# Kernel optimization log

Measured on AMD Instinct MI355X. Metric: run time of the kernel, lower is better.

The kernel has to match this reference:

```python
import math
import jax, jax.numpy as jnp
import numpy as np

D_MODEL = 256
D2 = 2 * D_MODEL
NHEADS = 8
NLAYERS = 6
FFN = 1024
Q, B, S = 300, 16, 1024


def _ln(x, eps=1e-5):
    m = jnp.mean(x, axis=-1, keepdims=True)
    v = jnp.mean((x - m) ** 2, axis=-1, keepdims=True)
    return (x - m) / jnp.sqrt(v + eps)


def _mlp2(x, W1, b1, W2, b2):
    return jnp.maximum(x @ W1 + b1, 0.0) @ W2 + b2


def _sine_embed(pos, d_model):
    # pos: [Q, B, 2] -> [Q, B, d_model]
    fd = d_model // 2
    dim_t = jnp.arange(fd, dtype=jnp.float32)
    dim_t = 10000.0 ** (2.0 * jnp.floor(dim_t / 2.0) / fd)
    scale = 2.0 * math.pi
    px = (pos[:, :, 0] * scale)[:, :, None] / dim_t
    py = (pos[:, :, 1] * scale)[:, :, None] / dim_t

    def inter(p):
        q, b, _ = p.shape
        return jnp.stack((jnp.sin(p[:, :, 0::2]), jnp.cos(p[:, :, 1::2])), axis=3).reshape(q, b, -1)

    return jnp.concatenate((inter(py), inter(px)), axis=2)


def _pairwise_iou(b):
    # b: [B, Q, 4] xyxy -> [B, Q, Q]
    area = (b[..., 2] - b[..., 0]) * (b[..., 3] - b[..., 1])
    lt = jnp.maximum(b[:, :, None, :2], b[:, None, :, :2])
    rb = jnp.minimum(b[:, :, None, 2:], b[:, None, :, 2:])
    wh = jnp.clip(rb - lt, 0.0)
    inter = wh[..., 0] * wh[..., 1]
    union = area[:, :, None] + area[:, None, :] - inter
    return inter / union


def _mha(q, k, v, Wq, Wk, Wv, Wo, bias=None):
    # q: [L,B,D], k/v: [S,B,D]
    L, Bb, D = q.shape
    Ss = k.shape[0]
    hd = D // NHEADS
    qh = (q @ Wq).reshape(L, Bb, NHEADS, hd).transpose(1, 2, 0, 3)  # [B,H,L,hd]
    kh = (k @ Wk).reshape(Ss, Bb, NHEADS, hd).transpose(1, 2, 0, 3)
    vh = (v @ Wv).reshape(Ss, Bb, NHEADS, hd).transpose(1, 2, 0, 3)
    logits = jnp.einsum('bhqd,bhkd->bhqk', qh, kh) / jnp.sqrt(jnp.float32(hd))
    if bias is not None:
        logits = logits + bias[:, None]  # broadcast over heads
    a = jax.nn.softmax(logits, axis=-1)
    o = jnp.einsum('bhqk,bhkd->bhqd', a, vh).transpose(2, 0, 1, 3).reshape(L, Bb, D)
    return o @ Wo


def setup_inputs() -> dict:
    key = jax.random.key(0)
    ks = iter(jax.random.split(key, 40))
    f32 = jnp.float32
    d = D_MODEL
    sc = 0.02
    inp = {
        'tgt': jax.random.normal(next(ks), (Q, B, D2), f32),
        'memory': jax.random.normal(next(ks), (S, B, D2), f32),
        'pos': jax.random.normal(next(ks), (S, B, D2), f32),
        'query_pos': jax.random.normal(next(ks), (Q, B, d), f32),
        # query_scale MLP (d->d->d)
        'qs_W1': jax.random.normal(next(ks), (d, d), f32) * sc, 'qs_b1': jnp.zeros((d,), f32),
        'qs_W2': jax.random.normal(next(ks), (d, d), f32) * sc, 'qs_b2': jnp.zeros((d,), f32),
        # ref_point_head MLP (d->d->2)
        'rp_W1': jax.random.normal(next(ks), (d, d), f32) * sc, 'rp_b1': jnp.zeros((d,), f32),
        'rp_W2': jax.random.normal(next(ks), (d, 2), f32) * sc, 'rp_b2': jnp.zeros((2,), f32),
        # bbox_embed_func MLP (d->d->4)
        'bb_W1': jax.random.normal(next(ks), (d, d), f32) * sc, 'bb_b1': jnp.zeros((d,), f32),
        'bb_W2': jax.random.normal(next(ks), (d, 4), f32) * sc, 'bb_b2': jnp.zeros((4,), f32),
    }
    for name in ['sa_Wq', 'sa_Wk', 'sa_Wv', 'sa_Wo', 'ca_Wq', 'ca_Wk', 'ca_Wv', 'ca_Wo']:
        inp[name] = jax.random.normal(next(ks), (NLAYERS, D2, D2), f32) * sc
    inp['ff_W1'] = jax.random.normal(next(ks), (NLAYERS, D2, FFN), f32) * sc
    inp['ff_b1'] = jnp.zeros((NLAYERS, FFN), f32)
    inp['ff_W2'] = jax.random.normal(next(ks), (NLAYERS, FFN, D2), f32) * sc
    inp['ff_b2'] = jnp.zeros((NLAYERS, D2), f32)
    return inp


def reference(tgt, memory, pos, query_pos,
              qs_W1, qs_b1, qs_W2, qs_b2,
              rp_W1, rp_b1, rp_W2, rp_b2,
              bb_W1, bb_b1, bb_W2, bb_b2,
              sa_Wq, sa_Wk, sa_Wv, sa_Wo,
              ca_Wq, ca_Wk, ca_Wv, ca_Wo,
              ff_W1, ff_b1, ff_W2, ff_b2):
    d = D_MODEL
    output = tgt
    ref_before = _mlp2(query_pos, rp_W1, rp_b1, rp_W2, rp_b2)          # [Q,B,2]
    reference_points = jax.nn.sigmoid(ref_before).transpose(1, 0, 2)   # [B,Q,2]
    qp2 = jnp.concatenate((query_pos, query_pos), axis=-1)             # [Q,B,2d]
    for l in range(NLAYERS):
        obj_center = reference_points.transpose(1, 0, 2)               # [Q,B,2]
        pos_transform = _mlp2(output[..., d:], qs_W1, qs_b1, qs_W2, qs_b2)
        qs = _sine_embed(obj_center, d) * pos_transform                # [Q,B,d]
        tmp = _mlp2(output[..., d:], bb_W1, bb_b1, bb_W2, bb_b2)       # [Q,B,4]
        tmp = tmp.at[..., :2].add(ref_before)
        coord = jax.nn.sigmoid(tmp)                                    # cxcywh
        cx, cy, w, h = coord[..., 0], coord[..., 1], coord[..., 2], coord[..., 3]
        boxes = jnp.stack((cx - 0.5 * w, cy - 0.5 * h, cx + 0.5 * w, cy + 0.5 * h),
                          axis=-1).transpose(1, 0, 2)                  # [B,Q,4]
        gious = jax.lax.stop_gradient(_pairwise_iou(boxes))            # [B,Q,Q]
        cs = (cx + cy).transpose(1, 0)                                 # [B,Q]
        cxcys = jax.lax.stop_gradient((cs[:, :, None] > cs[:, None, :]).astype(output.dtype))
        bias = gious + cxcys                                            # [B,Q,Q]
        qs2 = jnp.concatenate((qs, qs), axis=-1)                        # [Q,B,2d]
        # self-attention with giou/cxcy bias
        qsa = output + qp2
        sa = _mha(qsa, qsa, output, sa_Wq[l], sa_Wk[l], sa_Wv[l], sa_Wo[l], bias=bias)
        output = _ln(output + sa)
        # cross-attention, sine-modulated query
        ca = _mha(output + qp2 + qs2, memory + pos, memory,
                  ca_Wq[l], ca_Wk[l], ca_Wv[l], ca_Wo[l])
        output = _ln(output + ca)
        ff = jnp.maximum(output @ ff_W1[l] + ff_b1[l], 0.0) @ ff_W2[l] + ff_b2[l]
        output = _ln(output + ff)
    return output[None]  # [1,Q,B,2d]
```

## Files before the change

kernel.cpp:

```cpp
#include <hip/hip_runtime.h>
#include <cmath>

#define QLEN 300
#define BATCH 16
#define SLEN 1024
#define DM 256
#define DD 512
#define FFND 1024
#define NQROWS (QLEN*BATCH)
#define NMROWS (SLEN*BATCH)
#define LQPAD 304
#define SAKPAD 320

typedef __attribute__((ext_vector_type(8))) short short8;
typedef __attribute__((ext_vector_type(4))) float f32x4;
typedef __attribute__((ext_vector_type(4))) unsigned short ushort4_;

__device__ __forceinline__ float sigmoidf_(float x){ return 1.f/(1.f+expf(-x)); }

__device__ __forceinline__ unsigned short f2bf(float x){
  unsigned u = __float_as_uint(x);
  unsigned r = (u + 0x7FFFu + ((u >> 16) & 1u)) >> 16;
  return (unsigned short)r;
}
__device__ __forceinline__ float bf2f(unsigned short u){
  return __uint_as_float(((unsigned)u) << 16);
}

__device__ __forceinline__ void gload16(const void* g, void* l) {
  __builtin_amdgcn_global_load_lds((const __attribute__((address_space(1))) unsigned int*)g,
                                   (__attribute__((address_space(3))) unsigned int*)l, 16, 0, 0);
}

__global__ __launch_bounds__(256) void transpose_cvt(
    const float* __restrict__ W, unsigned short* __restrict__ Wt, int K, int N,
    size_t zsrc, size_t zdst, float scale)
{
  __shared__ float T[32][33];
  int n0 = blockIdx.x*32, k0 = blockIdx.y*32;
  size_t zs = (size_t)blockIdx.z * zsrc;
  size_t zd = (size_t)blockIdx.z * zdst;
  int tx = threadIdx.x & 31, ty = threadIdx.x >> 5;
  #pragma unroll
  for (int j = 0; j < 32; j += 8)
    T[ty+j][tx] = W[zs + (size_t)(k0+ty+j)*N + n0+tx];
  __syncthreads();
  #pragma unroll
  for (int j = 0; j < 32; j += 8)
    Wt[zd + (size_t)(n0+ty+j)*K + k0+tx] = f2bf(T[tx][ty+j] * scale);
}

__global__ void concat_bias(const float* __restrict__ b1, const float* __restrict__ b2,
                            float* __restrict__ out)
{
  int i = blockIdx.x*256 + threadIdx.x;
  if (i < 256) out[i] = b1[i];
  else if (i < 512) out[i] = b2[i-256];
}

template<int BM, int OUTMODE, bool RELU>
__global__ __launch_bounds__(256) void gemm2(
    const unsigned short* __restrict__ Ab, const unsigned short* __restrict__ Wt,
    const float* __restrict__ bias, void* __restrict__ Cptr,
    int M, int N, int K, int lda, int Laux)
{
  __shared__ __align__(16) unsigned short As[2][BM*64];
  __shared__ __align__(16) unsigned short Bs[2][128*64];
  const int tid = threadIdx.x;
  const int w = tid >> 6, lane = tid & 63;
  const int bm = blockIdx.y*BM, bn = blockIdx.x*128;
  const int wm = w >> 1, wn = w & 1;
  const int c = lane & 15, hi = lane >> 4;
  constexpr int MR = (BM + 31)/32 < 1 ? 1 : BM/32;
  f32x4 acc[MR < 1 ? 1 : MR][4] = {};
  const int lrow8 = lane >> 3;
  const int lcol  = ((lane & 7) ^ lrow8) << 3;
  const int nt = K >> 6;

  auto stage = [&](int buf, int k0) {
    #pragma unroll
    for (int it = 0; it < BM/32; ++it) {
      int r = it*32 + w*8;
      gload16(&Ab[(size_t)(bm + r + lrow8)*lda + k0 + lcol], &As[buf][r*64]);
    }
    #pragma unroll
    for (int it = 0; it < 4; ++it) {
      int r = it*32 + w*8;
      gload16(&Wt[(size_t)(bn + r + lrow8)*K + k0 + lcol], &Bs[buf][r*64]);
    }
  };

  stage(0, 0);
  for (int t = 0; t < nt; ++t) {
    const int cur = t & 1;
    if (t + 1 < nt) {
      stage(cur ^ 1, (t+1) << 6);
      if constexpr (BM == 32)      asm volatile("s_waitcnt vmcnt(5)" ::: "memory");
      else if constexpr (BM == 64) asm volatile("s_waitcnt vmcnt(6)" ::: "memory");
      else                         asm volatile("s_waitcnt vmcnt(8)" ::: "memory");
    } else {
      asm volatile("s_waitcnt vmcnt(0)" ::: "memory");
    }
    __builtin_amdgcn_s_barrier();
    #pragma unroll
    for (int ks = 0; ks < 2; ++ks) {
      short8 a[MR], bf[4];
      #pragma unroll
      for (int mr = 0; mr < MR; ++mr) {
        int m = wm*(BM/2) + mr*16 + c;
        a[mr] = *reinterpret_cast<const short8*>(&As[cur][m*64 + ((ks*32 + hi*8) ^ ((m&7)<<3))]);
      }
      #pragma unroll
      for (int nr = 0; nr < 4; ++nr) {
        int n = wn*64 + nr*16 + c;
        bf[nr] = *reinterpret_cast<const short8*>(&Bs[cur][n*64 + ((ks*32 + hi*8) ^ ((n&7)<<3))]);
      }
      #pragma unroll
      for (int mr = 0; mr < MR; ++mr)
        #pragma unroll
        for (int nr = 0; nr < 4; ++nr)
          acc[mr][nr] = __builtin_amdgcn_mfma_f32_16x16x32_bf16(a[mr], bf[nr], acc[mr][nr], 0, 0, 0);
    }
    asm volatile("s_waitcnt lgkmcnt(0)" ::: "memory");
    __builtin_amdgcn_sched_barrier(0);
    __builtin_amdgcn_s_barrier();
  }
  const int hs = N >> 6;
  #pragma unroll
  for (int mr = 0; mr < MR; ++mr) {
    #pragma unroll
    for (int nr = 0; nr < 4; ++nr) {
      int colg = bn + wn*64 + nr*16 + c;
      float bv = bias ? bias[colg] : 0.f;
      #pragma unroll
      for (int r = 0; r < 4; ++r) {
        int rowg = bm + wm*(BM/2) + mr*16 + hi*4 + r;
        float v = acc[mr][nr][r] + bv;
        if (RELU) v = fmaxf(v, 0.f);
        if (OUTMODE == 0) {
          ((float*)Cptr)[(size_t)rowg*N + colg] = v;
        } else if (OUTMODE == 1) {
          ((unsigned short*)Cptr)[(size_t)rowg*N + colg] = f2bf(v);
        } else {
          int bb = rowg & 15, row = rowg >> 4, h = colg >> 6, dl = colg & 63;
          ((unsigned short*)Cptr)[(((size_t)bb*hs + h)*Laux + row)*64 + dl] = f2bf(v);
        }
      }
    }
  }
}

template<int BM>
__global__ __launch_bounds__(256) void gemm2_vt(
    const unsigned short* __restrict__ Ab, const unsigned short* __restrict__ Wt,
    unsigned short* __restrict__ VT, int Lsrc, int K, int lda, int Lkpad, int tilesPerB)
{
  __shared__ __align__(16) unsigned short As[2][BM*64];
  __shared__ __align__(16) unsigned short Bs[2][128*64];
  const int tid = threadIdx.x;
  const int w = tid >> 6, lane = tid & 63;
  const int b = blockIdx.y / tilesPerB;
  const int qt = (blockIdx.y - b*tilesPerB) * BM;
  const int bn = blockIdx.x*128;
  const int wm = w >> 1, wn = w & 1;
  const int c = lane & 15, hi = lane >> 4;
  constexpr int MR = BM/32;
  f32x4 acc[MR][4] = {};
  const int lrow8 = lane >> 3;
  const int lcol  = ((lane & 7) ^ lrow8) << 3;
  const int nt = K >> 6;

  auto stage = [&](int buf, int k0) {
    #pragma unroll
    for (int it = 0; it < BM/32; ++it) {
      int r = it*32 + w*8;
      int q = qt + r + lrow8; if (q > Lsrc-1) q = Lsrc-1;
      gload16(&Ab[(size_t)(q*BATCH + b)*lda + k0 + lcol], &As[buf][r*64]);
    }
    #pragma unroll
    for (int it = 0; it < 4; ++it) {
      int r = it*32 + w*8;
      gload16(&Wt[(size_t)(bn + r + lrow8)*K + k0 + lcol], &Bs[buf][r*64]);
    }
  };

  stage(0, 0);
  for (int t = 0; t < nt; ++t) {
    const int cur = t & 1;
    if (t + 1 < nt) {
      stage(cur ^ 1, (t+1) << 6);
      if constexpr (BM == 64) asm volatile("s_waitcnt vmcnt(6)" ::: "memory");
      else                    asm volatile("s_waitcnt vmcnt(8)" ::: "memory");
    } else {
      asm volatile("s_waitcnt vmcnt(0)" ::: "memory");
    }
    __builtin_amdgcn_s_barrier();
    #pragma unroll
    for (int ks = 0; ks < 2; ++ks) {
      short8 a[MR], bf[4];
      #pragma unroll
      for (int mr = 0; mr < MR; ++mr) {
        int m = wm*(BM/2) + mr*16 + c;
        a[mr] = *reinterpret_cast<const short8*>(&As[cur][m*64 + ((ks*32 + hi*8) ^ ((m&7)<<3))]);
      }
      #pragma unroll
      for (int nr = 0; nr < 4; ++nr) {
        int n = wn*64 + nr*16 + c;
        bf[nr] = *reinterpret_cast<const short8*>(&Bs[cur][n*64 + ((ks*32 + hi*8) ^ ((n&7)<<3))]);
      }
      #pragma unroll
      for (int mr = 0; mr < MR; ++mr)
        #pragma unroll
        for (int nr = 0; nr < 4; ++nr)
          acc[mr][nr] = __builtin_amdgcn_mfma_f32_16x16x32_bf16(a[mr], bf[nr], acc[mr][nr], 0, 0, 0);
    }
    asm volatile("s_waitcnt lgkmcnt(0)" ::: "memory");
    __builtin_amdgcn_sched_barrier(0);
    __builtin_amdgcn_s_barrier();
  }
  #pragma unroll
  for (int mr = 0; mr < MR; ++mr) {
    #pragma unroll
    for (int nr = 0; nr < 4; ++nr) {
      int colg = bn + wn*64 + nr*16 + c;
      int h = colg >> 6, dl = colg & 63;
      int q0 = qt + wm*(BM/2) + mr*16 + hi*4;
      ushort4_ pack;
      #pragma unroll
      for (int r = 0; r < 4; ++r) pack[r] = f2bf(acc[mr][nr][r]);
      *reinterpret_cast<ushort4_*>(&VT[((size_t)(b*8 + h)*64 + dl)*Lkpad + q0]) = pack;
    }
  }
}

__global__ __launch_bounds__(256) void gemm_mfma_split(
    const unsigned short* __restrict__ Ab, const unsigned short* __restrict__ Wt,
    const float* __restrict__ bias, unsigned short* __restrict__ C1, float* __restrict__ C2,
    int M, int N, int K, int lda)
{
  __shared__ __align__(16) unsigned short As[64][72];
  __shared__ __align__(16) unsigned short Bs[64][72];
  const int tid = threadIdx.x;
  const int bm = blockIdx.y*64, bn = blockIdx.x*64;
  const int w = tid >> 6, lane = tid & 63;
  const int wm = w >> 1, wn = w & 1;
  const int c = lane & 15, hi = lane >> 4;
  const int sr = tid >> 3, sk = (tid & 7) * 8;
  f32x4 acc[2][2] = {};
  for (int k0 = 0; k0 < K; k0 += 64) {
    #pragma unroll
    for (int it = 0; it < 2; ++it) {
      int m = sr + it*32;
      short8 v = *reinterpret_cast<const short8*>(&Ab[(size_t)(bm+m)*lda + k0 + sk]);
      *reinterpret_cast<short8*>(&As[m][sk]) = v;
      short8 bv = *reinterpret_cast<const short8*>(&Wt[(size_t)(bn+m)*K + k0 + sk]);
      *reinterpret_cast<short8*>(&Bs[m][sk]) = bv;
    }
    __syncthreads();
    #pragma unroll
    for (int ks = 0; ks < 2; ++ks) {
      short8 a0 = *reinterpret_cast<const short8*>(&As[wm*32 + c][ks*32 + hi*8]);
      short8 a1 = *reinterpret_cast<const short8*>(&As[wm*32 + 16 + c][ks*32 + hi*8]);
      short8 b0 = *reinterpret_cast<const short8*>(&Bs[wn*32 + c][ks*32 + hi*8]);
      short8 b1 = *reinterpret_cast<const short8*>(&Bs[wn*32 + 16 + c][ks*32 + hi*8]);
      acc[0][0] = __builtin_amdgcn_mfma_f32_16x16x32_bf16(a0, b0, acc[0][0], 0, 0, 0);
      acc[0][1] = __builtin_amdgcn_mfma_f32_16x16x32_bf16(a0, b1, acc[0][1], 0, 0, 0);
      acc[1][0] = __builtin_amdgcn_mfma_f32_16x16x32_bf16(a1, b0, acc[1][0], 0, 0, 0);
      acc[1][1] = __builtin_amdgcn_mfma_f32_16x16x32_bf16(a1, b1, acc[1][1], 0, 0, 0);
    }
    __syncthreads();
  }
  #pragma unroll
  for (int mf = 0; mf < 2; ++mf) {
    #pragma unroll
    for (int nf = 0; nf < 2; ++nf) {
      int colg = bn + wn*32 + nf*16 + c;
      float bv = bias[colg];
      #pragma unroll
      for (int r = 0; r < 4; ++r) {
        int rowg = bm + wm*32 + mf*16 + hi*4 + r;
        float v = fmaxf(acc[mf][nf][r] + bv, 0.f);
        if (colg < 256) C1[(size_t)rowg*256 + colg] = f2bf(v);
        else            C2[(size_t)rowg*256 + (colg-256)] = v;
      }
    }
  }
}

template<bool HAS_BIAS, bool MASK, int NS>
__global__ __launch_bounds__(256) void attn2(
    const unsigned short* __restrict__ Qh, const unsigned short* __restrict__ Kh,
    const unsigned short* __restrict__ VT, const float* __restrict__ bias,
    unsigned short* __restrict__ Ob, unsigned short* __restrict__ Opart, float* __restrict__ MLpart,
    int Lq, int Lk, int Lkpad, int qmul, int kmul, int koff)
{
  __shared__ __align__(16) unsigned short Ks[2][64*64];
  __shared__ __align__(16) unsigned short Vs[2][64*64];
  __shared__ __align__(16) unsigned short Pl[4][16][72];
  const int tid = threadIdx.x;
  const int w = tid >> 6, lane = tid & 63;
  const int c = lane & 15, hi = lane >> 4;
  const int bh = blockIdx.x;
  const int qt = blockIdx.y * 64;
  const int sp = blockIdx.z;
  const int b = bh >> 3, h = bh & 7;
  const int lrow8 = lane >> 3;
  const int lcol  = ((lane & 7) ^ lrow8) << 3;

  const int nt_tot = (Lk + 63) >> 6;
  const int t0 = (nt_tot * sp) / NS;
  const int t1 = (nt_tot * (sp + 1)) / NS;

  int qrow = qt + w*16 + c; if (qrow > Lq-1) qrow = Lq-1;
  const unsigned short* qptr = Qh + ((size_t)(b*qmul + h)*Lq + qrow)*64;
  short8 qf0 = *reinterpret_cast<const short8*>(qptr + hi*8);
  short8 qf1 = *reinterpret_cast<const short8*>(qptr + 32 + hi*8);
  const size_t kbase = (size_t)(b*kmul + koff + h)*Lk;

  float m_ = -1e30f, l_ = 0.f;
  f32x4 accO[4] = {};
  const int qbase = qt + w*16 + hi*4;

  auto stageKV = [&](int buf, int kt) {
    #pragma unroll
    for (int it = 0; it < 2; ++it) {
      int r = it*32 + w*8;
      int kr = kt + r + lrow8; if (MASK && kr > Lk-1) kr = Lk-1;
      gload16(&Kh[(kbase + kr)*64 + lcol], &Ks[buf][r*64]);
    }
    #pragma unroll
    for (int it = 0; it < 2; ++it) {
      int r = it*32 + w*8;
      gload16(&VT[((size_t)bh*64 + r + lrow8)*Lkpad + kt + lcol], &Vs[buf][r*64]);
    }
  };

  stageKV(0, t0 << 6);
  for (int t = t0; t < t1; ++t) {
    const int cur = (t - t0) & 1;
    const int kt = t << 6;
    float4 bs4[4];
    if (HAS_BIAS) {
      #pragma unroll
      for (int g = 0; g < 4; ++g)
        bs4[g] = *reinterpret_cast<const float4*>(
            &bias[((size_t)b*Lq + qrow)*Lk + kt + g*16 + hi*4]);
    }
    if (t + 1 < t1) {
      stageKV(cur ^ 1, (t+1) << 6);
      asm volatile("s_waitcnt vmcnt(4)" ::: "memory");
    } else {
      asm volatile("s_waitcnt vmcnt(0)" ::: "memory");
    }
    __builtin_amdgcn_s_barrier();
    f32x4 s[4] = {};
    __builtin_amdgcn_s_setprio(1);
    #pragma unroll
    for (int g = 0; g < 4; ++g) {
      int m = g*16 + c;
      short8 kb0 = *reinterpret_cast<const short8*>(&Ks[cur][m*64 + ((hi*8)      ^ ((m&7)<<3))]);
      short8 kb1 = *reinterpret_cast<const short8*>(&Ks[cur][m*64 + ((32 + hi*8) ^ ((m&7)<<3))]);
      s[g] = __builtin_amdgcn_mfma_f32_16x16x32_bf16(kb0, qf0, s[g], 0, 0, 0);
      s[g] = __builtin_amdgcn_mfma_f32_16x16x32_bf16(kb1, qf1, s[g], 0, 0, 0);
    }
    __builtin_amdgcn_s_setprio(0);
    float tmax = -1e30f;
    #pragma unroll
    for (int g = 0; g < 4; ++g) {
      #pragma unroll
      for (int r = 0; r < 4; ++r) {
        float v = s[g][r];
        if (HAS_BIAS) v += ((const float*)&bs4[g])[r];
        if (MASK && (kt + g*16 + hi*4 + r >= Lk)) v = -1e30f;
        s[g][r] = v;
        tmax = fmaxf(tmax, v);
      }
    }
    tmax = fmaxf(tmax, __shfl_xor(tmax, 16));
    tmax = fmaxf(tmax, __shfl_xor(tmax, 32));
    if (!__all(tmax - m_ <= 8.f)) {
      float newm = fmaxf(m_, tmax);
      float corr = __expf(m_ - newm);
      m_ = newm;
      l_ *= corr;
      float corr4[4];
      #pragma unroll
      for (int r = 0; r < 4; ++r) corr4[r] = __shfl(corr, hi*4 + r);
      #pragma unroll
      for (int dg = 0; dg < 4; ++dg)
        #pragma unroll
        for (int r = 0; r < 4; ++r) accO[dg][r] *= corr4[r];
    }
    float psum = 0.f;
    #pragma unroll
    for (int g = 0; g < 4; ++g) {
      ushort4_ pp;
      #pragma unroll
      for (int r = 0; r < 4; ++r) {
        float e = __expf(s[g][r] - m_);
        psum += e;
        pp[r] = f2bf(e);
      }
      *reinterpret_cast<ushort4_*>(&Pl[w][c][g*16 + hi*4]) = pp;
    }
    psum += __shfl_xor(psum, 16);
    psum += __shfl_xor(psum, 32);
    l_ += psum;
    __builtin_amdgcn_s_setprio(1);
    #pragma unroll
    for (int ks = 0; ks < 2; ++ks) {
      short8 pa = *reinterpret_cast<const short8*>(&Pl[w][c][ks*32 + hi*8]);
      #pragma unroll
      for (int dg = 0; dg < 4; ++dg) {
        int n = dg*16 + c;
        short8 vb = *reinterpret_cast<const short8*>(&Vs[cur][n*64 + ((ks*32 + hi*8) ^ ((n&7)<<3))]);
        accO[dg] = __builtin_amdgcn_mfma_f32_16x16x32_bf16(pa, vb, accO[dg], 0, 0, 0);
      }
    }
    __builtin_amdgcn_s_setprio(0);
    asm volatile("s_waitcnt lgkmcnt(0)" ::: "memory");
    __builtin_amdgcn_sched_barrier(0);
    __builtin_amdgcn_s_barrier();
  }
  if (NS == 1) {
    float l4[4];
    #pragma unroll
    for (int r = 0; r < 4; ++r) l4[r] = __shfl(l_, hi*4 + r);
    #pragma unroll
    for (int r = 0; r < 4; ++r) {
      int qg = qbase + r;
      if (qg < Lq) {
        float inv = 1.f / l4[r];
        #pragma unroll
        for (int dg = 0; dg < 4; ++dg)
          Ob[((size_t)qg*BATCH + b)*DD + h*64 + 16*dg + c] = f2bf(accO[dg][r] * inv);
      }
    }
  } else {
    int qc = qt + w*16 + c;
    if (hi == 0 && qc < Lq) {
      size_t rowml = ((size_t)sp*128 + bh)*LQPAD + qc;
      MLpart[rowml*2]     = m_;
      MLpart[rowml*2 + 1] = l_;
    }
    #pragma unroll
    for (int r = 0; r < 4; ++r) {
      int qg = qbase + r;
      if (qg < Lq) {
        size_t rowo = ((size_t)sp*128 + bh)*LQPAD + qg;
        #pragma unroll
        for (int dg = 0; dg < 4; ++dg)
          Opart[rowo*64 + dg*16 + c] = f2bf(accO[dg][r]);
      }
    }
  }
}

__global__ __launch_bounds__(256) void attn_reduce(
    const unsigned short* __restrict__ Opart, const float* __restrict__ MLpart,
    unsigned short* __restrict__ Ob, int Lq)
{
  int w = threadIdx.x >> 6, lane = threadIdx.x & 63;
  int pair = blockIdx.x*4 + w;
  if (pair >= 128*Lq) return;
  int bh = pair / Lq, q = pair - bh*Lq;
  size_t r0 = (size_t)bh*LQPAD + q;
  size_t r1 = (size_t)(128 + bh)*LQPAD + q;
  float m0 = MLpart[r0*2], l0 = MLpart[r0*2+1];
  float m1 = MLpart[r1*2], l1 = MLpart[r1*2+1];
  float M = fmaxf(m0, m1);
  float w0 = __expf(m0 - M), w1 = __expf(m1 - M);
  float o = w0*bf2f(Opart[r0*64 + lane]) + w1*bf2f(Opart[r1*64 + lane]);
  float l = w0*l0 + w1*l1;
  int b = bh >> 3, h = bh & 7;
  Ob[((size_t)q*BATCH + b)*DD + h*64 + lane] = f2bf(o / l);
}

__global__ __launch_bounds__(256) void gemm_f32(
    const float* __restrict__ A, const float* __restrict__ A2,
    const float* __restrict__ W, const float* __restrict__ bias,
    float* __restrict__ C, int M, int N, int K, int lda, int relu)
{
  __shared__ __align__(16) float As[16][68];
  __shared__ __align__(16) float Bs[16][68];
  const int tid = threadIdx.x;
  const int bm = blockIdx.y * 64, bn = blockIdx.x * 64;
  const int tx = tid & 15, ty = tid >> 4;
  const int ar = tid >> 4, ac = tid & 15;
  const int bk = tid >> 6, bnn = tid & 63;
  float acc[4][4] = {};
  for (int k0 = 0; k0 < K; k0 += 16) {
    #pragma unroll
    for (int i = 0; i < 4; ++i) {
      int row = ar + i*16;
      float v = A[(size_t)(bm+row)*lda + (k0+ac)];
      if (A2) v += A2[(size_t)(bm+row)*lda + (k0+ac)];
      As[ac][row] = v;
    }
    #pragma unroll
    for (int i = 0; i < 4; ++i) {
      int kk = bk + i*4;
      Bs[kk][bnn] = W[(size_t)(k0+kk)*N + (bn+bnn)];
    }
    __syncthreads();
    #pragma unroll
    for (int k = 0; k < 16; ++k) {
      float4 a4 = *reinterpret_cast<const float4*>(&As[k][ty*4]);
      float4 b4 = *reinterpret_cast<const float4*>(&Bs[k][tx*4]);
      float a[4] = {a4.x,a4.y,a4.z,a4.w};
      float bb[4] = {b4.x,b4.y,b4.z,b4.w};
      #pragma unroll
      for (int i=0;i<4;++i)
        #pragma unroll
        for (int j=0;j<4;++j)
          acc[i][j] = fmaf(a[i], bb[j], acc[i][j]);
    }
    __syncthreads();
  }
  float vb[4] = {0.f,0.f,0.f,0.f};
  if (bias) {
    float4 b4 = *reinterpret_cast<const float4*>(&bias[bn + tx*4]);
    vb[0]=b4.x; vb[1]=b4.y; vb[2]=b4.z; vb[3]=b4.w;
  }
  #pragma unroll
  for (int i=0;i<4;++i) {
    int row = bm + ty*4 + i;
    float r0 = acc[i][0]+vb[0], r1 = acc[i][1]+vb[1], r2 = acc[i][2]+vb[2], r3 = acc[i][3]+vb[3];
    if (relu){ r0=fmaxf(r0,0.f); r1=fmaxf(r1,0.f); r2=fmaxf(r2,0.f); r3=fmaxf(r3,0.f); }
    float4 o; o.x=r0; o.y=r1; o.z=r2; o.w=r3;
    *reinterpret_cast<float4*>(&C[(size_t)row*N + bn + tx*4]) = o;
  }
}

__global__ __launch_bounds__(256) void gemm_skinny(
    const float* __restrict__ A, const float* __restrict__ W, const float* __restrict__ bias,
    float* __restrict__ C, int M, int N, int K, int lda)
{
  int wid = threadIdx.x >> 6, lane = threadIdx.x & 63;
  int row = blockIdx.x * 4 + wid;
  if (row >= M) return;
  float acc[4] = {0.f,0.f,0.f,0.f};
  for (int k = lane; k < K; k += 64) {
    float av = A[(size_t)row*lda + k];
    for (int n = 0; n < N; ++n) acc[n] += av * W[(size_t)k*N + n];
  }
  for (int off = 32; off; off >>= 1)
    for (int n = 0; n < N; ++n) acc[n] += __shfl_down(acc[n], off);
  if (lane == 0)
    for (int n = 0; n < N; ++n) C[(size_t)row*N + n] = acc[n] + bias[n];
}

__global__ void sine_embed_kernel(const float* __restrict__ refb, float* __restrict__ sine)
{
  int idx = blockIdx.x*blockDim.x + threadIdx.x;
  if (idx >= NQROWS*DM) return;
  int r = idx >> 8, c = idx & 255;
  int j = c & 127;
  float coord = refb[r*2 + (c < 128 ? 1 : 0)];
  float s = sigmoidf_(coord);
  float freq = expf(-(float)(j >> 1) * (9.210340371976184f / 64.f));
  float v = s * 6.283185307179586f * freq;
  sine[idx] = (j & 1) ? cosf(v) : sinf(v);
}

__global__ void boxes_kernel(const float* __restrict__ t4, const float* __restrict__ refb,
                             float* __restrict__ boxes, float* __restrict__ cs)
{
  int idx = blockIdx.x*blockDim.x + threadIdx.x;
  if (idx >= NQROWS) return;
  int q = idx / BATCH, b = idx % BATCH;
  float cx = sigmoidf_(t4[idx*4+0] + refb[idx*2+0]);
  float cy = sigmoidf_(t4[idx*4+1] + refb[idx*2+1]);
  float w  = sigmoidf_(t4[idx*4+2]);
  float h  = sigmoidf_(t4[idx*4+3]);
  int o = b*QLEN + q;
  boxes[o*4+0] = cx - 0.5f*w;
  boxes[o*4+1] = cy - 0.5f*h;
  boxes[o*4+2] = cx + 0.5f*w;
  boxes[o*4+3] = cy + 0.5f*h;
  cs[o] = cx + cy;
}

__global__ void bias_kernel(const float* __restrict__ boxes, const float* __restrict__ cs,
                            float* __restrict__ bias)
{
  int idx = blockIdx.x*blockDim.x + threadIdx.x;
  const int QQ = QLEN*QLEN;
  if (idx >= BATCH*QQ) return;
  int b = idx / QQ, rem = idx - b*QQ;
  int i = rem / QLEN, j = rem - i*QLEN;
  float4 bi = *reinterpret_cast<const float4*>(&boxes[((size_t)b*QLEN + i)*4]);
  float4 bj = *reinterpret_cast<const float4*>(&boxes[((size_t)b*QLEN + j)*4]);
  float ai = (bi.z-bi.x)*(bi.w-bi.y);
  float aj = (bj.z-bj.x)*(bj.w-bj.y);
  float ltx = fmaxf(bi.x, bj.x), lty = fmaxf(bi.y, bj.y);
  float rbx = fminf(bi.z, bj.z), rby = fminf(bi.w, bj.w);
  float w = fmaxf(rbx-ltx, 0.f), h = fmaxf(rby-lty, 0.f);
  float inter = w*h;
  float iou = inter / (ai + aj - inter);
  bias[idx] = iou + ((cs[b*QLEN+i] > cs[b*QLEN+j]) ? 1.f : 0.f);
}

__global__ void cvt_mem(const float* __restrict__ mem, const float* __restrict__ pos,
                        unsigned short* __restrict__ mb, unsigned short* __restrict__ mvb)
{
  int i = blockIdx.x*blockDim.x + threadIdx.x;
  if (i >= NMROWS*DD/8) return;
  size_t base = (size_t)i*8;
  float4 a0 = *reinterpret_cast<const float4*>(mem+base);
  float4 a1 = *reinterpret_cast<const float4*>(mem+base+4);
  float4 p0 = *reinterpret_cast<const float4*>(pos+base);
  float4 p1 = *reinterpret_cast<const float4*>(pos+base+4);
  short8 s1, s2;
  s1[0]=(short)f2bf(a0.x+p0.x); s1[1]=(short)f2bf(a0.y+p0.y); s1[2]=(short)f2bf(a0.z+p0.z); s1[3]=(short)f2bf(a0.w+p0.w);
  s1[4]=(short)f2bf(a1.x+p1.x); s1[5]=(short)f2bf(a1.y+p1.y); s1[6]=(short)f2bf(a1.z+p1.z); s1[7]=(short)f2bf(a1.w+p1.w);
  s2[0]=(short)f2bf(a0.x); s2[1]=(short)f2bf(a0.y); s2[2]=(short)f2bf(a0.z); s2[3]=(short)f2bf(a0.w);
  s2[4]=(short)f2bf(a1.x); s2[5]=(short)f2bf(a1.y); s2[6]=(short)f2bf(a1.z); s2[7]=(short)f2bf(a1.w);
  *reinterpret_cast<short8*>(mb+base)  = s1;
  *reinterpret_cast<short8*>(mvb+base) = s2;
}

template<int EMIT>
__global__ __launch_bounds__(256) void ln_residual_t(
    float* __restrict__ X, const float* __restrict__ Y, unsigned short* __restrict__ Xb,
    const float* __restrict__ qp, const float* __restrict__ sine, const float* __restrict__ pt,
    unsigned short* __restrict__ QIN)
{
  int row = blockIdx.x, tid = threadIdx.x;
  size_t base = (size_t)row*DD;
  float v0 = X[base+tid]     + Y[base+tid];
  float v1 = X[base+tid+256] + Y[base+tid+256];
  float s = v0+v1, sq = v0*v0+v1*v1;
  for (int off = 32; off; off >>= 1) { s += __shfl_down(s,off); sq += __shfl_down(sq,off); }
  __shared__ float ss[4], ssq[4];
  int wid = tid>>6, lane = tid&63;
  if (lane==0){ ss[wid]=s; ssq[wid]=sq; }
  __syncthreads();
  if (tid==0){
    float a=ss[0]+ss[1]+ss[2]+ss[3], bsum=ssq[0]+ssq[1]+ssq[2]+ssq[3];
    float mean = a*(1.f/DD);
    float var  = bsum*(1.f/DD) - mean*mean;
    ss[0]=mean; ssq[0]=rsqrtf(fmaxf(var,0.f)+1e-5f);
  }
  __syncthreads();
  float mean = ss[0], inv = ssq[0];
  float o0 = (v0-mean)*inv, o1 = (v1-mean)*inv;
  X[base+tid]     = o0;  Xb[base+tid]     = f2bf(o0);
  X[base+tid+256] = o1;  Xb[base+tid+256] = f2bf(o1);
  if (EMIT >= 1) {
    size_t c2 = (size_t)row*256 + tid;
    float add = qp[c2];
    if (EMIT == 2) add += sine[c2]*pt[c2];
    QIN[base+tid]     = f2bf(o0 + add);
    QIN[base+tid+256] = f2bf(o1 + add);
  }
}

__global__ void init_x(const float* __restrict__ t, const float* __restrict__ qp,
                       float* __restrict__ X, unsigned short* __restrict__ Xb,
                       unsigned short* __restrict__ QIN, int n)
{
  int idx = blockIdx.x*blockDim.x + threadIdx.x;
  if (idx < n){
    float v = t[idx]; X[idx]=v; Xb[idx]=f2bf(v);
    int r = idx >> 9, c = idx & 511;
    QIN[idx] = f2bf(v + qp[(r<<8) + (c & 255)]);
  }
}

__global__ void copy_f32(const float* __restrict__ src, float* __restrict__ dst, int n)
{
  int idx = blockIdx.x*blockDim.x + threadIdx.x;
  if (idx < n) dst[idx] = src[idx];
}

extern "C" void kernel_launch(void* const* d_in, const int* in_sizes, int n_in,
                              void* d_out, int out_size, void* d_ws, size_t ws_size,
                              hipStream_t stream)
{
  const float* tgt       = (const float*)d_in[0];
  const float* memory    = (const float*)d_in[1];
  const float* pos       = (const float*)d_in[2];
  const float* query_pos = (const float*)d_in[3];
  const float* qs_W1 = (const float*)d_in[4];  const float* qs_b1 = (const float*)d_in[5];
  const float* qs_W2 = (const float*)d_in[6];  const float* qs_b2 = (const float*)d_in[7];
  const float* rp_W1 = (const float*)d_in[8];  const float* rp_b1 = (const float*)d_in[9];
  const float* rp_W2 = (const float*)d_in[10]; const float* rp_b2 = (const float*)d_in[11];
  const float* bb_W1 = (const float*)d_in[12]; const float* bb_b1 = (const float*)d_in[13];
  const float* bb_W2 = (const float*)d_in[14]; const float* bb_b2 = (const float*)d_in[15];
  const float* sa_Wq = (const float*)d_in[16]; const float* sa_Wk = (const float*)d_in[17];
  const float* sa_Wv = (const float*)d_in[18]; const float* sa_Wo = (const float*)d_in[19];
  const float* ca_Wq = (const float*)d_in[20]; const float* ca_Wk = (const float*)d_in[21];
  const float* ca_Wv = (const float*)d_in[22]; const float* ca_Wo = (const float*)d_in[23];
  const float* ff_W1 = (const float*)d_in[24]; const float* ff_b1 = (const float*)d_in[25];
  const float* ff_W2 = (const float*)d_in[26]; const float* ff_b2 = (const float*)d_in[27];

  float* F = (float*)d_ws;
  size_t o = 0;
  float* X    = F + o; o += (size_t)NQROWS*DD;
  float* RES  = F + o; o += (size_t)NQROWS*DD;
  float* SINE = F + o; o += (size_t)NQROWS*DM;
  float* PT   = F + o; o += (size_t)NQROWS*DM;
  float* BIAS = F + o; o += (size_t)BATCH*QLEN*QLEN;
  float* REFB = F + o; o += (size_t)NQROWS*2;
  float* T4   = F + o; o += (size_t)NQROWS*4;
  float* BOX  = F + o; o += (size_t)NQROWS*4;
  float* CS   = F + o; o += (size_t)NQROWS;
  float* ML   = F + o; o += (size_t)2*128*LQPAD*2;
  float* QBB  = F + o; o += 512;
  float* T256 = RES;
  unsigned short* U = (unsigned short*)(F + o);
  size_t u = 0;
  unsigned short* Xb   = U + u; u += (size_t)NQROWS*DD;
  unsigned short* QIN  = U + u; u += (size_t)NQROWS*DD;
  unsigned short* PQb  = U + u; u += (size_t)NQROWS*DD;
  unsigned short* PKb  = U + u; u += (size_t)NMROWS*DD;
  unsigned short* PVb  = U + u; u += (size_t)NMROWS*DD;
  unsigned short* VTsa = U + u; u += (size_t)128*64*SAKPAD;
  unsigned short* OPARTU = U + u; u += (size_t)2*128*LQPAD*64;
  unsigned short* T256b= U + u; u += (size_t)NQROWS*DM;
  unsigned short* MEMb = U + u; u += (size_t)NMROWS*DD;
  unsigned short* MEMVb= U + u; u += (size_t)NMROWS*DD;
  unsigned short* WtSqk= U + u; u += (size_t)6*2*DD*DD;
  unsigned short* WtSv = U + u; u += (size_t)6*DD*DD;
  unsigned short* WtSo = U + u; u += (size_t)6*DD*DD;
  unsigned short* WtCq = U + u; u += (size_t)6*DD*DD;
  unsigned short* WtCk = U + u; u += (size_t)6*DD*DD;
  unsigned short* WtCv = U + u; u += (size_t)6*DD*DD;
  unsigned short* WtCo = U + u; u += (size_t)6*DD*DD;
  unsigned short* WtF1 = U + u; u += (size_t)6*DD*FFND;
  unsigned short* WtF2 = U + u; u += (size_t)6*DD*FFND;
  unsigned short* WtQB = U + u; u += (size_t)2*DM*DM;
  unsigned short* WtQ2 = U + u; u += (size_t)DM*DM;
  unsigned short* QKb  = PQb;
  unsigned short* AOb  = QIN;
  unsigned short* HIDb = PKb;
  if (ws_size < o*sizeof(float) + u*sizeof(unsigned short)) return;

  dim3 B256(256);
  const int nTotal = NQROWS*DD;
  const size_t ZD = (size_t)DD*DD;
  const size_t ZM = (size_t)DM*DM;

  transpose_cvt<<<dim3(16,16,6), B256, 0, stream>>>(sa_Wq, WtSqk,      DD, DD, ZD, 2*ZD, 0.125f);
  transpose_cvt<<<dim3(16,16,6), B256, 0, stream>>>(sa_Wk, WtSqk + ZD, DD, DD, ZD, 2*ZD, 1.f);
  transpose_cvt<<<dim3(16,16,6), B256, 0, stream>>>(sa_Wv, WtSv, DD, DD, ZD, ZD, 1.f);
  transpose_cvt<<<dim3(16,16,6), B256, 0, stream>>>(sa_Wo, WtSo, DD, DD, ZD, ZD, 1.f);
  transpose_cvt<<<dim3(16,16,6), B256, 0, stream>>>(ca_Wq, WtCq, DD, DD, ZD, ZD, 0.125f);
  transpose_cvt<<<dim3(16,16,6), B256, 0, stream>>>(ca_Wk, WtCk, DD, DD, ZD, ZD, 1.f);
  transpose_cvt<<<dim3(16,16,6), B256, 0, stream>>>(ca_Wv, WtCv, DD, DD, ZD, ZD, 1.f);
  transpose_cvt<<<dim3(16,16,6), B256, 0, stream>>>(ca_Wo, WtCo, DD, DD, ZD, ZD, 1.f);
  transpose_cvt<<<dim3(32,16,6), B256, 0, stream>>>(ff_W1, WtF1, DD, FFND, (size_t)DD*FFND, (size_t)DD*FFND, 1.f);
  transpose_cvt<<<dim3(16,32,6), B256, 0, stream>>>(ff_W2, WtF2, FFND, DD, (size_t)DD*FFND, (size_t)DD*FFND, 1.f);
  transpose_cvt<<<dim3(8,8,1),  B256, 0, stream>>>(qs_W1, WtQB,      DM, DM, ZM, ZM, 1.f);
  transpose_cvt<<<dim3(8,8,1),  B256, 0, stream>>>(bb_W1, WtQB + ZM, DM, DM, ZM, ZM, 1.f);
  transpose_cvt<<<dim3(8,8,1),  B256, 0, stream>>>(qs_W2, WtQ2, DM, DM, ZM, ZM, 1.f);
  concat_bias<<<dim3(2), B256, 0, stream>>>(qs_b1, bb_b1, QBB);

  init_x<<<dim3((nTotal+255)/256), B256, 0, stream>>>(tgt, query_pos, X, Xb, QIN, nTotal);
  cvt_mem<<<dim3(NMROWS*DD/8/256), B256, 0, stream>>>(memory, pos, MEMb, MEMVb);
  gemm_f32<<<dim3(DM/64, NQROWS/64), B256, 0, stream>>>(query_pos, nullptr, rp_W1, rp_b1, T256, NQROWS, DM, DM, DM, 1);
  gemm_skinny<<<dim3(NQROWS/4), B256, 0, stream>>>(T256, rp_W2, rp_b2, REFB, NQROWS, 2, DM, DM);
  sine_embed_kernel<<<dim3((NQROWS*DM+255)/256), B256, 0, stream>>>(REFB, SINE);

  const int nredu = (128*QLEN + 3) / 4;
  const int qtiles = (QLEN + 63) / 64;
  for (int l = 0; l < 6; ++l) {
    const size_t wo = (size_t)l*DD*DD, fo = (size_t)l*DD*FFND;
    const float* fb1 = ff_b1 + (size_t)l*FFND;
    const float* fb2 = ff_b2 + (size_t)l*DD;

    gemm_mfma_split<<<dim3(8, NQROWS/64), B256, 0, stream>>>(Xb+DM, WtQB, QBB, T256b, T256, NQROWS, 512, DM, DD);
    gemm2<32,0,false><<<dim3(DM/128, NQROWS/32), B256, 0, stream>>>(T256b, WtQ2, qs_b2, PT, NQROWS, DM, DM, DM, 0);
    gemm_skinny<<<dim3(NQROWS/4), B256, 0, stream>>>(T256, bb_W2, bb_b2, T4, NQROWS, 4, DM, DM);
    boxes_kernel<<<dim3((NQROWS+255)/256), B256, 0, stream>>>(T4, REFB, BOX, CS);
    bias_kernel<<<dim3((BATCH*QLEN*QLEN+255)/256), B256, 0, stream>>>(BOX, CS, BIAS);

    gemm2<64,2,false><<<dim3(1024/128, NQROWS/64), B256, 0, stream>>>(QIN, WtSqk + (size_t)l*2*ZD, nullptr, QKb, NQROWS, 1024, DD, DD, QLEN);
    gemm2_vt<64><<<dim3(DD/128, BATCH*5), B256, 0, stream>>>(Xb, WtSv+wo, VTsa, QLEN, DD, DD, SAKPAD, 5);
    attn2<true,true,2><<<dim3(128, qtiles, 2), B256, 0, stream>>>(QKb, QKb, VTsa, BIAS, nullptr, OPARTU, ML, QLEN, QLEN, SAKPAD, 16, 16, 8);
    attn_reduce<<<dim3(nredu), B256, 0, stream>>>(OPARTU, ML, AOb, QLEN);
    gemm2<32,0,false><<<dim3(DD/128, NQROWS/32), B256, 0, stream>>>(AOb, WtSo+wo, nullptr, RES, NQROWS, DD, DD, DD, 0);
    ln_residual_t<2><<<dim3(NQROWS), B256, 0, stream>>>(X, RES, Xb, query_pos, SINE, PT, QIN);

    gemm2<32,2,false><<<dim3(DD/128, NQROWS/32), B256, 0, stream>>>(QIN, WtCq+wo, nullptr, PQb, NQROWS, DD, DD, DD, QLEN);
    gemm2<128,2,false><<<dim3(DD/128, NMROWS/128), B256, 0, stream>>>(MEMb,  WtCk+wo, nullptr, PKb, NMROWS, DD, DD, DD, SLEN);
    gemm2_vt<128><<<dim3(DD/128, BATCH*8), B256, 0, stream>>>(MEMVb, WtCv+wo, PVb, SLEN, DD, DD, SLEN, 8);
    attn2<false,false,2><<<dim3(128, qtiles, 2), B256, 0, stream>>>(PQb, PKb, PVb, nullptr, nullptr, OPARTU, ML, QLEN, SLEN, SLEN, 8, 8, 0);
    attn_reduce<<<dim3(nredu), B256, 0, stream>>>(OPARTU, ML, AOb, QLEN);
    gemm2<32,0,false><<<dim3(DD/128, NQROWS/32), B256, 0, stream>>>(AOb, WtCo+wo, nullptr, RES, NQROWS, DD, DD, DD, 0);
    ln_residual_t<0><<<dim3(NQROWS), B256, 0, stream>>>(X, RES, Xb, nullptr, nullptr, nullptr, nullptr);

    gemm2<64,1,true ><<<dim3(FFND/128, NQROWS/64), B256, 0, stream>>>(Xb, WtF1+fo, fb1, HIDb, NQROWS, FFND, DD, DD, 0);
    gemm2<32,0,false><<<dim3(DD/128, NQROWS/32), B256, 0, stream>>>(HIDb, WtF2+fo, fb2, RES, NQROWS, DD, FFND, FFND, 0);
    ln_residual_t<1><<<dim3(NQROWS), B256, 0, stream>>>(X, RES, Xb, query_pos, nullptr, nullptr, QIN);
  }

  copy_f32<<<dim3((nTotal+255)/256), B256, 0, stream>>>(X, (float*)d_out, out_size);
}
```

Before: 1.585 ms.

## Split cross-attention over four key chunks, swizzle P tile, shrink K/V GEMM tiles

```diff
diff --git a/kernel.cpp b/kernel.cpp
--- a/kernel.cpp
+++ b/kernel.cpp
@@ -11,6 +11,7 @@
 #define NMROWS (SLEN*BATCH)
 #define LQPAD 304
 #define SAKPAD 320
+#define NSCA 4
 
 typedef __attribute__((ext_vector_type(8))) short short8;
 typedef __attribute__((ext_vector_type(4))) float f32x4;
@@ -296,7 +297,7 @@
 {
   __shared__ __align__(16) unsigned short Ks[2][64*64];
   __shared__ __align__(16) unsigned short Vs[2][64*64];
-  __shared__ __align__(16) unsigned short Pl[4][16][72];
+  __shared__ __align__(16) unsigned short Pl[4][16*64];
   const int tid = threadIdx.x;
   const int w = tid >> 6, lane = tid & 63;
   const int c = lane & 15, hi = lane >> 4;
@@ -401,7 +402,8 @@
         psum += e;
         pp[r] = f2bf(e);
       }
-      *reinterpret_cast<ushort4_*>(&Pl[w][c][g*16 + hi*4]) = pp;
+      int idx = c*64 + ((((g<<1)|(hi>>1)) ^ (c&7))<<3) + ((hi&1)<<2);
+      *reinterpret_cast<ushort4_*>(&Pl[w][idx]) = pp;
     }
     psum += __shfl_xor(psum, 16);
     psum += __shfl_xor(psum, 32);
@@ -409,7 +411,7 @@
     __builtin_amdgcn_s_setprio(1);
     #pragma unroll
     for (int ks = 0; ks < 2; ++ks) {
-      short8 pa = *reinterpret_cast<const short8*>(&Pl[w][c][ks*32 + hi*8]);
+      short8 pa = *reinterpret_cast<const short8*>(&Pl[w][c*64 + ((((ks<<2)|hi) ^ (c&7))<<3)]);
       #pragma unroll
       for (int dg = 0; dg < 4; ++dg) {
         int n = dg*16 + c;
@@ -456,6 +458,7 @@
   }
 }
 
+template<int NSR>
 __global__ __launch_bounds__(256) void attn_reduce(
     const unsigned short* __restrict__ Opart, const float* __restrict__ MLpart,
     unsigned short* __restrict__ Ob, int Lq)
@@ -464,16 +467,24 @@
   int pair = blockIdx.x*4 + w;
   if (pair >= 128*Lq) return;
   int bh = pair / Lq, q = pair - bh*Lq;
-  size_t r0 = (size_t)bh*LQPAD + q;
-  size_t r1 = (size_t)(128 + bh)*LQPAD + q;
-  float m0 = MLpart[r0*2], l0 = MLpart[r0*2+1];
-  float m1 = MLpart[r1*2], l1 = MLpart[r1*2+1];
-  float M = fmaxf(m0, m1);
-  float w0 = __expf(m0 - M), w1 = __expf(m1 - M);
-  float o = w0*bf2f(Opart[r0*64 + lane]) + w1*bf2f(Opart[r1*64 + lane]);
-  float l = w0*l0 + w1*l1;
+  size_t rr[NSR];
+  float m[NSR], l[NSR], M = -1e30f;
+  #pragma unroll
+  for (int s = 0; s < NSR; ++s) {
+    rr[s] = ((size_t)s*128 + bh)*LQPAD + q;
+    m[s] = MLpart[rr[s]*2];
+    l[s] = MLpart[rr[s]*2 + 1];
+    M = fmaxf(M, m[s]);
+  }
+  float o = 0.f, L = 0.f;
+  #pragma unroll
+  for (int s = 0; s < NSR; ++s) {
+    float wg = __expf(m[s] - M);
+    o += wg * bf2f(Opart[rr[s]*64 + lane]);
+    L += wg * l[s];
+  }
   int b = bh >> 3, h = bh & 7;
-  Ob[((size_t)q*BATCH + b)*DD + h*64 + lane] = f2bf(o / l);
+  Ob[((size_t)q*BATCH + b)*DD + h*64 + lane] = f2bf(o / L);
 }
 
 __global__ __launch_bounds__(256) void gemm_f32(
@@ -706,7 +717,7 @@
   float* T4   = F + o; o += (size_t)NQROWS*4;
   float* BOX  = F + o; o += (size_t)NQROWS*4;
   float* CS   = F + o; o += (size_t)NQROWS;
-  float* ML   = F + o; o += (size_t)2*128*LQPAD*2;
+  float* ML   = F + o; o += (size_t)NSCA*128*LQPAD*2;
   float* QBB  = F + o; o += 512;
   float* T256 = RES;
   unsigned short* U = (unsigned short*)(F + o);
@@ -717,7 +728,7 @@
   unsigned short* PKb  = U + u; u += (size_t)NMROWS*DD;
   unsigned short* PVb  = U + u; u += (size_t)NMROWS*DD;
   unsigned short* VTsa = U + u; u += (size_t)128*64*SAKPAD;
-  unsigned short* OPARTU = U + u; u += (size_t)2*128*LQPAD*64;
+  unsigned short* OPARTU = U + u; u += (size_t)NSCA*128*LQPAD*64;
   unsigned short* T256b= U + u; u += (size_t)NQROWS*DM;
   unsigned short* MEMb = U + u; u += (size_t)NMROWS*DD;
   unsigned short* MEMVb= U + u; u += (size_t)NMROWS*DD;
@@ -779,15 +790,15 @@
     gemm2<64,2,false><<<dim3(1024/128, NQROWS/64), B256, 0, stream>>>(QIN, WtSqk + (size_t)l*2*ZD, nullptr, QKb, NQROWS, 1024, DD, DD, QLEN);
     gemm2_vt<64><<<dim3(DD/128, BATCH*5), B256, 0, stream>>>(Xb, WtSv+wo, VTsa, QLEN, DD, DD, SAKPAD, 5);
     attn2<true,true,2><<<dim3(128, qtiles, 2), B256, 0, stream>>>(QKb, QKb, VTsa, BIAS, nullptr, OPARTU, ML, QLEN, QLEN, SAKPAD, 16, 16, 8);
-    attn_reduce<<<dim3(nredu), B256, 0, stream>>>(OPARTU, ML, AOb, QLEN);
+    attn_reduce<2><<<dim3(nredu), B256, 0, stream>>>(OPARTU, ML, AOb, QLEN);
     gemm2<32,0,false><<<dim3(DD/128, NQROWS/32), B256, 0, stream>>>(AOb, WtSo+wo, nullptr, RES, NQROWS, DD, DD, DD, 0);
     ln_residual_t<2><<<dim3(NQROWS), B256, 0, stream>>>(X, RES, Xb, query_pos, SINE, PT, QIN);
 
     gemm2<32,2,false><<<dim3(DD/128, NQROWS/32), B256, 0, stream>>>(QIN, WtCq+wo, nullptr, PQb, NQROWS, DD, DD, DD, QLEN);
-    gemm2<128,2,false><<<dim3(DD/128, NMROWS/128), B256, 0, stream>>>(MEMb,  WtCk+wo, nullptr, PKb, NMROWS, DD, DD, DD, SLEN);
-    gemm2_vt<128><<<dim3(DD/128, BATCH*8), B256, 0, stream>>>(MEMVb, WtCv+wo, PVb, SLEN, DD, DD, SLEN, 8);
-    attn2<false,false,2><<<dim3(128, qtiles, 2), B256, 0, stream>>>(PQb, PKb, PVb, nullptr, nullptr, OPARTU, ML, QLEN, SLEN, SLEN, 8, 8, 0);
-    attn_reduce<<<dim3(nredu), B256, 0, stream>>>(OPARTU, ML, AOb, QLEN);
+    gemm2<64,2,false><<<dim3(DD/128, NMROWS/64), B256, 0, stream>>>(MEMb,  WtCk+wo, nullptr, PKb, NMROWS, DD, DD, DD, SLEN);
+    gemm2_vt<64><<<dim3(DD/128, BATCH*16), B256, 0, stream>>>(MEMVb, WtCv+wo, PVb, SLEN, DD, DD, SLEN, 16);
+    attn2<false,false,NSCA><<<dim3(128, qtiles, NSCA), B256, 0, stream>>>(PQb, PKb, PVb, nullptr, nullptr, OPARTU, ML, QLEN, SLEN, SLEN, 8, 8, 0);
+    attn_reduce<NSCA><<<dim3(nredu), B256, 0, stream>>>(OPARTU, ML, AOb, QLEN);
     gemm2<32,0,false><<<dim3(DD/128, NQROWS/32), B256, 0, stream>>>(AOb, WtCo+wo, nullptr, RES, NQROWS, DD, DD, DD, 0);
     ln_residual_t<0><<<dim3(NQROWS), B256, 0, stream>>>(X, RES, Xb, nullptr, nullptr, nullptr, nullptr);
 
```

Measured after the change: 1.612 ms. About the same (+1.7%).
